# Kernel optimization log

Measured on AMD Instinct MI355X. Metric: run time of the kernel, lower is better.

## Reference

```python
import jax, jax.numpy as jnp
import numpy as np

B, LQ, LK, D = 4, 256, 256, 768


def setup_inputs() -> dict:
    key = jax.random.key(0)
    ks = jax.random.split(key, 11)
    s = 1.0 / np.sqrt(D)
    return {
        "query": jax.random.normal(ks[0], (B, LQ, D), jnp.float32),
        "key": jax.random.normal(ks[1], (B, LK, D), jnp.float32),
        "value": jax.random.normal(ks[2], (B, LK, D), jnp.float32),
        "Wq": jax.random.uniform(ks[3], (D, D), jnp.float32, -s, s),
        "bq": jax.random.uniform(ks[4], (D,), jnp.float32, -s, s),
        "Wk": jax.random.uniform(ks[5], (D, D), jnp.float32, -s, s),
        "bk": jax.random.uniform(ks[6], (D,), jnp.float32, -s, s),
        "Wv": jax.random.uniform(ks[7], (D, D), jnp.float32, -s, s),
        "bv": jax.random.uniform(ks[8], (D,), jnp.float32, -s, s),
        "Ws": jax.random.uniform(ks[9], (D,), jnp.float32, -s, s),
        "bs": jax.random.uniform(ks[10], (), jnp.float32, -s, s),
    }


def reference(query, key, value, Wq, bq, Wk, bk, Wv, bv, Ws, bs):
    # Linear projections (torch Linear: x @ W.T + b; here W stored as [in, out])
    q = jnp.einsum('bqd,de->bqe', query, Wq) + bq   # [B,Lq,D]
    k = jnp.einsum('bkd,de->bke', key, Wk) + bk     # [B,Lk,D]
    v = jnp.einsum('bkd,de->bke', value, Wv) + bv   # [B,Lk,D]
    # Additive (Bahdanau) scores: tanh(q_i + k_j) . Ws + bs  -> [B,Lq,Lk]
    h = jnp.tanh(q[:, :, None, :] + k[:, None, :, :])  # [B,Lq,Lk,D]
    scores = jnp.einsum('bqkd,d->bqk', h, Ws) + bs
    attention_weights = jax.nn.softmax(scores, axis=-1)  # [B,Lq,Lk]
    attended = jnp.einsum('bqk,bkd->bqd', attention_weights, v)
    return attended, attention_weights
```

## Files before the change

kernel.cpp:

```cpp
#include <hip/hip_runtime.h>

#define NB 4
#define SLQ 256
#define SLK 256
#define DD 768

#define TWO_LOG2E 2.8853900817779268f
#define LOG2E 1.4426950408889634f

typedef _Float16 f16x4 __attribute__((ext_vector_type(4)));
typedef _Float16 f16x8 __attribute__((ext_vector_type(8)));
typedef float f32x4 __attribute__((ext_vector_type(4)));

__device__ __forceinline__ float fexp2(float x) { return __builtin_amdgcn_exp2f(x); }
__device__ __forceinline__ float frcp(float x) { return __builtin_amdgcn_rcpf(x); }

#define LSTR 40
#define TSTR 72
#define NPS  ((size_t)NB * SLQ * SLK)

__global__ __launch_bounds__(256) void prep_a_kernel(
    const float* __restrict__ q, const float* __restrict__ k,
    const float* __restrict__ v, _Float16* __restrict__ qh,
    _Float16* __restrict__ kh, _Float16* __restrict__ vh)
{
    const int z = blockIdx.z;
    const float* src = (z == 0) ? q : (z == 1) ? k : v;
    _Float16* dst = (z == 0) ? qh : (z == 1) ? kh : vh;
    const int i8 = (blockIdx.x * 256 + threadIdx.x) * 8;
    float4 a = *(const float4*)&src[i8];
    float4 b = *(const float4*)&src[i8 + 4];
    f16x8 h;
    h[0] = (_Float16)a.x; h[1] = (_Float16)a.y; h[2] = (_Float16)a.z; h[3] = (_Float16)a.w;
    h[4] = (_Float16)b.x; h[5] = (_Float16)b.y; h[6] = (_Float16)b.z; h[7] = (_Float16)b.w;
    *(f16x8*)&dst[i8] = h;
}

__global__ __launch_bounds__(256) void prep_wt_kernel(
    const float* __restrict__ Wq, const float* __restrict__ Wk,
    const float* __restrict__ Wv, _Float16* __restrict__ wtq,
    _Float16* __restrict__ wtk, _Float16* __restrict__ wtv)
{
    const int z = blockIdx.z;
    const float* W = (z == 0) ? Wq : (z == 1) ? Wk : Wv;
    _Float16* Wt = (z == 0) ? wtq : (z == 1) ? wtk : wtv;

    __shared__ float t[64][65];
    const int tid = threadIdx.x;
    const int kt0 = blockIdx.y * 64;
    const int nt0 = blockIdx.x * 64;

    const int col4 = (tid & 15) << 2;
#pragma unroll
    for (int i = 0; i < 4; ++i) {
        const int row = ((tid >> 4) << 2) + i;
        *(float4*)&t[row][col4] = *(const float4*)&W[(size_t)(kt0 + row) * DD + nt0 + col4];
    }
    __syncthreads();
    const int n = tid >> 2;
    const int k16 = (tid & 3) << 4;
    f16x8 h0, h1;
#pragma unroll
    for (int j = 0; j < 8; ++j) {
        h0[j] = (_Float16)t[k16 + j][n];
        h1[j] = (_Float16)t[k16 + 8 + j][n];
    }
    *(f16x8*)&Wt[(size_t)(nt0 + n) * DD + kt0 + k16] = h0;
    *(f16x8*)&Wt[(size_t)(nt0 + n) * DD + kt0 + k16 + 8] = h1;
}

__global__ __launch_bounds__(256) void qkv_f16_kernel(
    const _Float16* __restrict__ qh, const _Float16* __restrict__ kh,
    const _Float16* __restrict__ vh, const _Float16* __restrict__ wtq,
    const _Float16* __restrict__ wtk, const _Float16* __restrict__ wtv,
    const float* __restrict__ bq, const float* __restrict__ bk,
    const float* __restrict__ bv, float* __restrict__ eq,
    _Float16* __restrict__ ekc, _Float16* __restrict__ vsht)
{
    const int z = blockIdx.z;
    const _Float16* A = (z == 0) ? qh : (z == 1) ? kh : vh;
    const _Float16* Wt = (z == 0) ? wtq : (z == 1) ? wtk : wtv;
    const float* bias = (z == 0) ? bq : (z == 1) ? bk : bv;

    __shared__ _Float16 Sh[2][2][64 * LSTR];

    const int tid = threadIdx.x;
    const int lane = tid & 63;
    const int wid = tid >> 6;
    const int wr = wid >> 1;
    const int wc = wid & 1;
    const int row0 = blockIdx.y * 64;
    const int col0 = blockIdx.x * 64;

    const int sr = tid >> 2;
    const int sc = (tid & 3) << 3;

    const _Float16* Ap = A + (size_t)(row0 + sr) * DD + sc;
    const _Float16* Bp = Wt + (size_t)(col0 + sr) * DD + sc;

    f16x8 pa = *(const f16x8*)Ap;
    f16x8 pb = *(const f16x8*)Bp;

    f32x4 acc[2][2] = {};
    const int kj = (lane >> 4) << 3;
    const int fr = lane & 15;

    *(f16x8*)&Sh[0][0][sr * LSTR + sc] = pa;
    *(f16x8*)&Sh[0][1][sr * LSTR + sc] = pb;
    __syncthreads();

    int p = 0;
    for (int s = 0; s < DD / 32; ++s) {
        if (s + 1 < DD / 32) {
            pa = *(const f16x8*)(Ap + (s + 1) * 32);
            pb = *(const f16x8*)(Bp + (s + 1) * 32);
        }
        f16x8 af0 = *(const f16x8*)&Sh[p][0][(wr * 32 + fr) * LSTR + kj];
        f16x8 af1 = *(const f16x8*)&Sh[p][0][(wr * 32 + 16 + fr) * LSTR + kj];
        f16x8 bf0 = *(const f16x8*)&Sh[p][1][(wc * 32 + fr) * LSTR + kj];
        f16x8 bf1 = *(const f16x8*)&Sh[p][1][(wc * 32 + 16 + fr) * LSTR + kj];
        acc[0][0] = __builtin_amdgcn_mfma_f32_16x16x32_f16(af0, bf0, acc[0][0], 0, 0, 0);
        acc[0][1] = __builtin_amdgcn_mfma_f32_16x16x32_f16(af0, bf1, acc[0][1], 0, 0, 0);
        acc[1][0] = __builtin_amdgcn_mfma_f32_16x16x32_f16(af1, bf0, acc[1][0], 0, 0, 0);
        acc[1][1] = __builtin_amdgcn_mfma_f32_16x16x32_f16(af1, bf1, acc[1][1], 0, 0, 0);
        if (s + 1 < DD / 32) {
            *(f16x8*)&Sh[p ^ 1][0][sr * LSTR + sc] = pa;
            *(f16x8*)&Sh[p ^ 1][1][sr * LSTR + sc] = pb;
        }
        __syncthreads();
        p ^= 1;
    }

    const int colb = col0 + wc * 32 + fr;
    const int rowb = row0 + wr * 32 + ((lane >> 4) << 2);

    if (z < 2) {
#pragma unroll
        for (int mf = 0; mf < 2; ++mf) {
#pragma unroll
            for (int nf = 0; nf < 2; ++nf) {
                const int col = colb + nf * 16;
                const float bvv = bias[col];
#pragma unroll
                for (int r = 0; r < 4; ++r) {
                    const int row = rowb + mf * 16 + r;
                    const float arg = fminf((acc[mf][nf][r] + bvv) * TWO_LOG2E, 15.0f);
                    if (z == 0) {
                        eq[(size_t)row * DD + col] = fexp2(arg);
                    } else {
                        const int b = row >> 8, k = row & 255;
                        ekc[(size_t)b * (SLK * DD) + ((col >> 3) * (SLK * 8)) +
                            k * 8 + (col & 7)] = (_Float16)fexp2(arg);
                    }
                }
            }
        }
    } else {
        _Float16* T = (_Float16*)Sh;
#pragma unroll
        for (int mf = 0; mf < 2; ++mf) {
#pragma unroll
            for (int nf = 0; nf < 2; ++nf) {
                const int cl = wc * 32 + fr + nf * 16;
                const float bvv = bias[col0 + cl];
                const int rl = wr * 32 + mf * 16 + ((lane >> 4) << 2);
                f16x4 h;
#pragma unroll
                for (int r = 0; r < 4; ++r) h[r] = (_Float16)(acc[mf][nf][r] + bvv);
                *(f16x4*)&T[cl * TSTR + rl] = h;
            }
        }
        __syncthreads();
        const int b = row0 >> 8;
        const int krow0 = row0 & 255;
#pragma unroll
        for (int j = 0; j < 2; ++j) {
            const int u = tid + 256 * j;
            const int c2 = u >> 3;
            const int g = u & 7;
            f16x8 hv = *(const f16x8*)&T[c2 * TSTR + g * 8];
            *(f16x8*)&vsht[((size_t)b * DD + col0 + c2) * SLK + krow0 + g * 8] = hv;
        }
    }
}

__global__ __launch_bounds__(256) void scores_partial_kernel(
    const float* __restrict__ Eq, const _Float16* __restrict__ Ekc,
    const float* __restrict__ Ws, float* __restrict__ pbuf)
{
    const int bz = blockIdx.z;
    const int b = bz >> 2;
    const int s = bz & 3;
    const int k0 = blockIdx.x * 64;
    const int q0 = blockIdx.y * 8;
    const int lane = threadIdx.x & 63;
    const int wid = __builtin_amdgcn_readfirstlane((int)(threadIdx.x >> 6));
    const int q = q0 + (wid << 1);
    const int d0 = s * 192;

    const _Float16* kr = Ekc + (size_t)b * (SLK * DD) + ((d0 >> 3) * (SLK * 8)) +
                         (k0 + lane) * 8;
    const float* qp0 = Eq + (size_t)(b * SLQ + q) * DD + d0;
    const float* qp1 = qp0 + DD;
    const float* wp = Ws + d0;

    float acc0 = 0.f, acc1 = 0.f;

#pragma unroll 4
    for (int c = 0; c < 24; ++c) {
        const int dn = c * 8;
        f16x8 e = *(const f16x8*)(kr + (size_t)c * (SLK * 8));
        float4 ga0 = *(const float4*)(qp0 + dn);
        float4 ga1 = *(const float4*)(qp0 + dn + 4);
        float4 gb0 = *(const float4*)(qp1 + dn);
        float4 gb1 = *(const float4*)(qp1 + dn + 4);
        float4 w0 = *(const float4*)(wp + dn);
        float4 w1 = *(const float4*)(wp + dn + 4);

        float e0 = (float)e[0], e1 = (float)e[1], e2 = (float)e[2], e3 = (float)e[3];
        float e4 = (float)e[4], e5 = (float)e[5], e6 = (float)e[6], e7 = (float)e[7];

        acc0 = fmaf(w0.x, frcp(fmaf(ga0.x, e0, 1.0f)), acc0);
        acc1 = fmaf(w0.x, frcp(fmaf(gb0.x, e0, 1.0f)), acc1);
        acc0 = fmaf(w0.y, frcp(fmaf(ga0.y, e1, 1.0f)), acc0);
        acc1 = fmaf(w0.y, frcp(fmaf(gb0.y, e1, 1.0f)), acc1);
        acc0 = fmaf(w0.z, frcp(fmaf(ga0.z, e2, 1.0f)), acc0);
        acc1 = fmaf(w0.z, frcp(fmaf(gb0.z, e2, 1.0f)), acc1);
        acc0 = fmaf(w0.w, frcp(fmaf(ga0.w, e3, 1.0f)), acc0);
        acc1 = fmaf(w0.w, frcp(fmaf(gb0.w, e3, 1.0f)), acc1);
        acc0 = fmaf(w1.x, frcp(fmaf(ga1.x, e4, 1.0f)), acc0);
        acc1 = fmaf(w1.x, frcp(fmaf(gb1.x, e4, 1.0f)), acc1);
        acc0 = fmaf(w1.y, frcp(fmaf(ga1.y, e5, 1.0f)), acc0);
        acc1 = fmaf(w1.y, frcp(fmaf(gb1.y, e5, 1.0f)), acc1);
        acc0 = fmaf(w1.z, frcp(fmaf(ga1.z, e6, 1.0f)), acc0);
        acc1 = fmaf(w1.z, frcp(fmaf(gb1.z, e6, 1.0f)), acc1);
        acc0 = fmaf(w1.w, frcp(fmaf(ga1.w, e7, 1.0f)), acc0);
        acc1 = fmaf(w1.w, frcp(fmaf(gb1.w, e7, 1.0f)), acc1);
    }

    const size_t o = (size_t)s * NPS + (size_t)(b * SLQ + q) * SLK + k0 + lane;
    pbuf[o] = -2.0f * acc0;
    pbuf[o + SLK] = -2.0f * acc1;
}

__global__ __launch_bounds__(256) void softmax_combine_kernel(
    const float* __restrict__ pbuf, float* __restrict__ attnw,
    _Float16* __restrict__ phalf)
{
    const int lane = threadIdx.x & 63;
    const int wv = threadIdx.x >> 6;
    const int row = blockIdx.x * 4 + wv;
    const size_t base = (size_t)row * SLK + (lane << 2);

    float4 x0 = *(const float4*)&pbuf[base];
    float4 x1 = *(const float4*)&pbuf[base + NPS];
    float4 x2 = *(const float4*)&pbuf[base + 2 * NPS];
    float4 x3 = *(const float4*)&pbuf[base + 3 * NPS];
    float4 x;
    x.x = (x0.x + x1.x) + (x2.x + x3.x);
    x.y = (x0.y + x1.y) + (x2.y + x3.y);
    x.z = (x0.z + x1.z) + (x2.z + x3.z);
    x.w = (x0.w + x1.w) + (x2.w + x3.w);

    float m = fmaxf(fmaxf(x.x, x.y), fmaxf(x.z, x.w));
#pragma unroll
    for (int off = 32; off; off >>= 1) m = fmaxf(m, __shfl_xor(m, off, 64));

    float e0 = fexp2((x.x - m) * LOG2E);
    float e1 = fexp2((x.y - m) * LOG2E);
    float e2 = fexp2((x.z - m) * LOG2E);
    float e3 = fexp2((x.w - m) * LOG2E);
    float sm = (e0 + e1) + (e2 + e3);
#pragma unroll
    for (int off = 32; off; off >>= 1) sm += __shfl_xor(sm, off, 64);

    const float inv = 1.0f / sm;
    float4 o;
    o.x = e0 * inv; o.y = e1 * inv; o.z = e2 * inv; o.w = e3 * inv;
    *(float4*)&attnw[base] = o;

    f16x4 h;
    h[0] = (_Float16)o.x; h[1] = (_Float16)o.y;
    h[2] = (_Float16)o.z; h[3] = (_Float16)o.w;
    *(f16x4*)&phalf[base] = h;
}

__global__ __launch_bounds__(256) void attended_f16_kernel(
    const _Float16* __restrict__ phalf, const _Float16* __restrict__ vsht,
    float* __restrict__ out)
{
    const int b = blockIdx.z;
    const _Float16* A = phalf + (size_t)b * SLQ * SLK;
    const _Float16* Bt = vsht + (size_t)b * DD * SLK;
    float* C = out + (size_t)b * SLQ * DD;

    __shared__ _Float16 Sh[2][2][64 * LSTR];

    const int tid = threadIdx.x;
    const int lane = tid & 63;
    const int wid = tid >> 6;
    const int wr = wid >> 1;
    const int wc = wid & 1;
    const int row0 = blockIdx.y * 64;
    const int col0 = blockIdx.x * 64;

    const int sr = tid >> 2;
    const int sc = (tid & 3) << 3;

    const _Float16* Ap = A + (size_t)(row0 + sr) * SLK + sc;
    const _Float16* Bp = Bt + (size_t)(col0 + sr) * SLK + sc;

    f16x8 pa = *(const f16x8*)Ap;
    f16x8 pb = *(const f16x8*)Bp;

    f32x4 acc[2][2] = {};
    const int kj = (lane >> 4) << 3;
    const int fr = lane & 15;

    *(f16x8*)&Sh[0][0][sr * LSTR + sc] = pa;
    *(f16x8*)&Sh[0][1][sr * LSTR + sc] = pb;
    __syncthreads();

    int p = 0;
    for (int s = 0; s < SLK / 32; ++s) {
        if (s + 1 < SLK / 32) {
            pa = *(const f16x8*)(Ap + (s + 1) * 32);
            pb = *(const f16x8*)(Bp + (s + 1) * 32);
        }
        f16x8 af0 = *(const f16x8*)&Sh[p][0][(wr * 32 + fr) * LSTR + kj];
        f16x8 af1 = *(const f16x8*)&Sh[p][0][(wr * 32 + 16 + fr) * LSTR + kj];
        f16x8 bf0 = *(const f16x8*)&Sh[p][1][(wc * 32 + fr) * LSTR + kj];
        f16x8 bf1 = *(const f16x8*)&Sh[p][1][(wc * 32 + 16 + fr) * LSTR + kj];
        acc[0][0] = __builtin_amdgcn_mfma_f32_16x16x32_f16(af0, bf0, acc[0][0], 0, 0, 0);
        acc[0][1] = __builtin_amdgcn_mfma_f32_16x16x32_f16(af0, bf1, acc[0][1], 0, 0, 0);
        acc[1][0] = __builtin_amdgcn_mfma_f32_16x16x32_f16(af1, bf0, acc[1][0], 0, 0, 0);
        acc[1][1] = __builtin_amdgcn_mfma_f32_16x16x32_f16(af1, bf1, acc[1][1], 0, 0, 0);
        if (s + 1 < SLK / 32) {
            *(f16x8*)&Sh[p ^ 1][0][sr * LSTR + sc] = pa;
            *(f16x8*)&Sh[p ^ 1][1][sr * LSTR + sc] = pb;
        }
        __syncthreads();
        p ^= 1;
    }

    const int colb = col0 + wc * 32 + fr;
    const int rowb = row0 + wr * 32 + ((lane >> 4) << 2);
#pragma unroll
    for (int mf = 0; mf < 2; ++mf)
#pragma unroll
        for (int nf = 0; nf < 2; ++nf)
#pragma unroll
            for (int r = 0; r < 4; ++r)
                C[(size_t)(rowb + mf * 16 + r) * DD + colb + nf * 16] = acc[mf][nf][r];
}

extern "C" void kernel_launch(void* const* d_in, const int* in_sizes, int n_in,
                              void* d_out, int out_size, void* d_ws, size_t ws_size,
                              hipStream_t stream)
{
    (void)in_sizes; (void)n_in; (void)out_size; (void)ws_size;

    const float* query = (const float*)d_in[0];
    const float* key   = (const float*)d_in[1];
    const float* value = (const float*)d_in[2];
    const float* Wq = (const float*)d_in[3];
    const float* bq = (const float*)d_in[4];
    const float* Wk = (const float*)d_in[5];
    const float* bk = (const float*)d_in[6];
    const float* Wv = (const float*)d_in[7];
    const float* bv = (const float*)d_in[8];
    const float* Ws = (const float*)d_in[9];

    const size_t NE = (size_t)NB * SLQ * DD;
    const size_t NW = (size_t)DD * DD;

    char* w = (char*)d_ws;
    float* eq = (float*)w;               w += NE * 4;
    _Float16* ekc = (_Float16*)w;        w += NE * 2;
    _Float16* vsht = (_Float16*)w;       w += NE * 2;
    _Float16* phalf = (_Float16*)w;      w += NPS * 2;
    _Float16* qh = (_Float16*)w;         w += NE * 2;
    _Float16* kh = (_Float16*)w;         w += NE * 2;
    _Float16* vh = (_Float16*)w;         w += NE * 2;
    _Float16* wtq = (_Float16*)w;        w += NW * 2;
    _Float16* wtk = (_Float16*)w;        w += NW * 2;
    _Float16* wtv = (_Float16*)w;        w += NW * 2;
    float* pbuf = (float*)w;

    float* out = (float*)d_out;
    float* attended = out;
    float* attnw = out + NE;

    prep_a_kernel<<<dim3(NE / (256 * 8), 1, 3), 256, 0, stream>>>(
        query, key, value, qh, kh, vh);
    prep_wt_kernel<<<dim3(DD / 64, DD / 64, 3), 256, 0, stream>>>(
        Wq, Wk, Wv, wtq, wtk, wtv);
    qkv_f16_kernel<<<dim3(DD / 64, (NB * SLQ) / 64, 3), 256, 0, stream>>>(
        qh, kh, vh, wtq, wtk, wtv, bq, bk, bv, eq, ekc, vsht);
    scores_partial_kernel<<<dim3(SLK / 64, SLQ / 8, NB * 4), 256, 0, stream>>>(
        eq, ekc, Ws, pbuf);
    softmax_combine_kernel<<<dim3((NB * SLQ) / 4), 256, 0, stream>>>(
        pbuf, attnw, phalf);
    attended_f16_kernel<<<dim3(DD / 64, SLQ / 64, NB), 256, 0, stream>>>(
        phalf, vsht, attended);
}
```

Baseline: 133.0 us.

## Fuse input fp16 conversion into QKV GEMM, stage epilogue, pair reciprocals, retile attended

Removes the separate input-to-fp16 prep kernel so the QKV GEMM loads fp32 inputs and converts them while staging into shared memory. The GEMM epilogue now writes through a shared-memory tile, giving coalesced vector stores for eq and the chunked ekc layout instead of scattered scalar stores. In the score kernel, pairs of reciprocals are merged into one reciprocal of a product, which roughly halves rcp instructions at the cost of extra multiplies and some overflow risk. The attended GEMM uses 64x32 tiles over a flattened batch so it launches more blocks.

```diff
diff --git a/kernel.cpp b/kernel.cpp
--- a/kernel.cpp
+++ b/kernel.cpp
@@ -17,24 +17,8 @@
 
 #define LSTR 40
 #define TSTR 72
+#define TFSTR 65
 #define NPS  ((size_t)NB * SLQ * SLK)
-
-__global__ __launch_bounds__(256) void prep_a_kernel(
-    const float* __restrict__ q, const float* __restrict__ k,
-    const float* __restrict__ v, _Float16* __restrict__ qh,
-    _Float16* __restrict__ kh, _Float16* __restrict__ vh)
-{
-    const int z = blockIdx.z;
-    const float* src = (z == 0) ? q : (z == 1) ? k : v;
-    _Float16* dst = (z == 0) ? qh : (z == 1) ? kh : vh;
-    const int i8 = (blockIdx.x * 256 + threadIdx.x) * 8;
-    float4 a = *(const float4*)&src[i8];
-    float4 b = *(const float4*)&src[i8 + 4];
-    f16x8 h;
-    h[0] = (_Float16)a.x; h[1] = (_Float16)a.y; h[2] = (_Float16)a.z; h[3] = (_Float16)a.w;
-    h[4] = (_Float16)b.x; h[5] = (_Float16)b.y; h[6] = (_Float16)b.z; h[7] = (_Float16)b.w;
-    *(f16x8*)&dst[i8] = h;
-}
 
 __global__ __launch_bounds__(256) void prep_wt_kernel(
     const float* __restrict__ Wq, const float* __restrict__ Wk,
@@ -70,15 +54,15 @@
 }
 
 __global__ __launch_bounds__(256) void qkv_f16_kernel(
-    const _Float16* __restrict__ qh, const _Float16* __restrict__ kh,
-    const _Float16* __restrict__ vh, const _Float16* __restrict__ wtq,
+    const float* __restrict__ query, const float* __restrict__ key_in,
+    const float* __restrict__ value, const _Float16* __restrict__ wtq,
     const _Float16* __restrict__ wtk, const _Float16* __restrict__ wtv,
     const float* __restrict__ bq, const float* __restrict__ bk,
     const float* __restrict__ bv, float* __restrict__ eq,
     _Float16* __restrict__ ekc, _Float16* __restrict__ vsht)
 {
     const int z = blockIdx.z;
-    const _Float16* A = (z == 0) ? qh : (z == 1) ? kh : vh;
+    const float* A = (z == 0) ? query : (z == 1) ? key_in : value;
     const _Float16* Wt = (z == 0) ? wtq : (z == 1) ? wtk : wtv;
     const float* bias = (z == 0) ? bq : (z == 1) ? bk : bv;
 
@@ -95,24 +79,33 @@
     const int sr = tid >> 2;
     const int sc = (tid & 3) << 3;
 
-    const _Float16* Ap = A + (size_t)(row0 + sr) * DD + sc;
+    const float* Ap = A + (size_t)(row0 + sr) * DD + sc;
     const _Float16* Bp = Wt + (size_t)(col0 + sr) * DD + sc;
 
-    f16x8 pa = *(const f16x8*)Ap;
+    float4 pa0 = *(const float4*)Ap;
+    float4 pa1 = *(const float4*)(Ap + 4);
     f16x8 pb = *(const f16x8*)Bp;
 
     f32x4 acc[2][2] = {};
     const int kj = (lane >> 4) << 3;
     const int fr = lane & 15;
 
-    *(f16x8*)&Sh[0][0][sr * LSTR + sc] = pa;
-    *(f16x8*)&Sh[0][1][sr * LSTR + sc] = pb;
+    {
+        f16x8 ha;
+        ha[0] = (_Float16)pa0.x; ha[1] = (_Float16)pa0.y;
+        ha[2] = (_Float16)pa0.z; ha[3] = (_Float16)pa0.w;
+        ha[4] = (_Float16)pa1.x; ha[5] = (_Float16)pa1.y;
+        ha[6] = (_Float16)pa1.z; ha[7] = (_Float16)pa1.w;
+        *(f16x8*)&Sh[0][0][sr * LSTR + sc] = ha;
+        *(f16x8*)&Sh[0][1][sr * LSTR + sc] = pb;
+    }
     __syncthreads();
 
     int p = 0;
     for (int s = 0; s < DD / 32; ++s) {
         if (s + 1 < DD / 32) {
-            pa = *(const f16x8*)(Ap + (s + 1) * 32);
+            pa0 = *(const float4*)(Ap + (s + 1) * 32);
+            pa1 = *(const float4*)(Ap + (s + 1) * 32 + 4);
             pb = *(const f16x8*)(Bp + (s + 1) * 32);
         }
         f16x8 af0 = *(const f16x8*)&Sh[p][0][(wr * 32 + fr) * LSTR + kj];
@@ -124,46 +117,72 @@
         acc[1][0] = __builtin_amdgcn_mfma_f32_16x16x32_f16(af1, bf0, acc[1][0], 0, 0, 0);
         acc[1][1] = __builtin_amdgcn_mfma_f32_16x16x32_f16(af1, bf1, acc[1][1], 0, 0, 0);
         if (s + 1 < DD / 32) {
-            *(f16x8*)&Sh[p ^ 1][0][sr * LSTR + sc] = pa;
+            f16x8 ha;
+            ha[0] = (_Float16)pa0.x; ha[1] = (_Float16)pa0.y;
+            ha[2] = (_Float16)pa0.z; ha[3] = (_Float16)pa0.w;
+            ha[4] = (_Float16)pa1.x; ha[5] = (_Float16)pa1.y;
+            ha[6] = (_Float16)pa1.z; ha[7] = (_Float16)pa1.w;
+            *(f16x8*)&Sh[p ^ 1][0][sr * LSTR + sc] = ha;
             *(f16x8*)&Sh[p ^ 1][1][sr * LSTR + sc] = pb;
         }
         __syncthreads();
         p ^= 1;
     }
 
-    const int colb = col0 + wc * 32 + fr;
-    const int rowb = row0 + wr * 32 + ((lane >> 4) << 2);
+    const int clb = wc * 32 + fr;
+    const int rlb = wr * 32 + ((lane >> 4) << 2);
 
     if (z < 2) {
+        float* Tf = (float*)Sh;
 #pragma unroll
         for (int mf = 0; mf < 2; ++mf) {
 #pragma unroll
             for (int nf = 0; nf < 2; ++nf) {
-                const int col = colb + nf * 16;
-                const float bvv = bias[col];
+                const int cl = clb + nf * 16;
+                const float bvv = bias[col0 + cl];
 #pragma unroll
                 for (int r = 0; r < 4; ++r) {
-                    const int row = rowb + mf * 16 + r;
+                    const int rl = rlb + mf * 16 + r;
                     const float arg = fminf((acc[mf][nf][r] + bvv) * TWO_LOG2E, 15.0f);
-                    if (z == 0) {
-                        eq[(size_t)row * DD + col] = fexp2(arg);
-                    } else {
-                        const int b = row >> 8, k = row & 255;
-                        ekc[(size_t)b * (SLK * DD) + ((col >> 3) * (SLK * 8)) +
-                            k * 8 + (col & 7)] = (_Float16)fexp2(arg);
-                    }
+                    Tf[rl * TFSTR + cl] = fexp2(arg);
                 }
             }
         }
+        __syncthreads();
+        if (z == 0) {
+#pragma unroll
+            for (int j = 0; j < 4; ++j) {
+                const int u = tid + j * 256;
+                const int row = u >> 4;
+                const int c4 = (u & 15) << 2;
+                float4 v = *(const float4*)&Tf[row * TFSTR + c4];
+                *(float4*)&eq[(size_t)(row0 + row) * DD + col0 + c4] = v;
+            }
+        } else {
+            const int b = row0 >> 8;
+            const int krow0 = row0 & 255;
+            const size_t base = (size_t)b * (SLK * DD) + (size_t)(col0 >> 3) * (SLK * 8);
+#pragma unroll
+            for (int j = 0; j < 2; ++j) {
+                const int u = tid + j * 256;
+                const int c2 = u >> 6;
+                const int k = u & 63;
+                const float* src = &Tf[k * TFSTR + c2 * 8];
+                f16x8 h;
+#pragma unroll
+                for (int i = 0; i < 8; ++i) h[i] = (_Float16)src[i];
+                *(f16x8*)&ekc[base + (size_t)c2 * (SLK * 8) + (size_t)(krow0 + k) * 8] = h;
+            }
+        }
     } else {
         _Float16* T = (_Float16*)Sh;
 #pragma unroll
         for (int mf = 0; mf < 2; ++mf) {
 #pragma unroll
             for (int nf = 0; nf < 2; ++nf) {
-                const int cl = wc * 32 + fr + nf * 16;
+                const int cl = clb + nf * 16;
                 const float bvv = bias[col0 + cl];
-                const int rl = wr * 32 + mf * 16 + ((lane >> 4) << 2);
+                const int rl = rlb + mf * 16;
                 f16x4 h;
 #pragma unroll
                 for (int r = 0; r < 4; ++r) h[r] = (_Float16)(acc[mf][nf][r] + bvv);
@@ -220,22 +239,26 @@
         float e0 = (float)e[0], e1 = (float)e[1], e2 = (float)e[2], e3 = (float)e[3];
         float e4 = (float)e[4], e5 = (float)e[5], e6 = (float)e[6], e7 = (float)e[7];
 
-        acc0 = fmaf(w0.x, frcp(fmaf(ga0.x, e0, 1.0f)), acc0);
-        acc1 = fmaf(w0.x, frcp(fmaf(gb0.x, e0, 1.0f)), acc1);
-        acc0 = fmaf(w0.y, frcp(fmaf(ga0.y, e1, 1.0f)), acc0);
-        acc1 = fmaf(w0.y, frcp(fmaf(gb0.y, e1, 1.0f)), acc1);
-        acc0 = fmaf(w0.z, frcp(fmaf(ga0.z, e2, 1.0f)), acc0);
-        acc1 = fmaf(w0.z, frcp(fmaf(gb0.z, e2, 1.0f)), acc1);
-        acc0 = fmaf(w0.w, frcp(fmaf(ga0.w, e3, 1.0f)), acc0);
-        acc1 = fmaf(w0.w, frcp(fmaf(gb0.w, e3, 1.0f)), acc1);
-        acc0 = fmaf(w1.x, frcp(fmaf(ga1.x, e4, 1.0f)), acc0);
-        acc1 = fmaf(w1.x, frcp(fmaf(gb1.x, e4, 1.0f)), acc1);
-        acc0 = fmaf(w1.y, frcp(fmaf(ga1.y, e5, 1.0f)), acc0);
-        acc1 = fmaf(w1.y, frcp(fmaf(gb1.y, e5, 1.0f)), acc1);
-        acc0 = fmaf(w1.z, frcp(fmaf(ga1.z, e6, 1.0f)), acc0);
-        acc1 = fmaf(w1.z, frcp(fmaf(gb1.z, e6, 1.0f)), acc1);
-        acc0 = fmaf(w1.w, frcp(fmaf(ga1.w, e7, 1.0f)), acc0);
-        acc1 = fmaf(w1.w, frcp(fmaf(gb1.w, e7, 1.0f)), acc1);
+        {
+            float A0 = fmaf(ga0.x, e0, 1.0f), A1 = fmaf(ga0.y, e1, 1.0f);
+            float A2 = fmaf(ga0.z, e2, 1.0f), A3 = fmaf(ga0.w, e3, 1.0f);
+            float A4 = fmaf(ga1.x, e4, 1.0f), A5 = fmaf(ga1.y, e5, 1.0f);
+            float A6 = fmaf(ga1.z, e6, 1.0f), A7 = fmaf(ga1.w, e7, 1.0f);
+            acc0 = fmaf(fmaf(w0.x, A1, w0.y * A0), frcp(A0 * A1), acc0);
+            acc0 = fmaf(fmaf(w0.z, A3, w0.w * A2), frcp(A2 * A3), acc0);
+            acc0 = fmaf(fmaf(w1.x, A5, w1.y * A4), frcp(A4 * A5), acc0);
+            acc0 = fmaf(fmaf(w1.z, A7, w1.w * A6), frcp(A6 * A7), acc0);
+        }
+        {
+            float A0 = fmaf(gb0.x, e0, 1.0f), A1 = fmaf(gb0.y, e1, 1.0f);
+            float A2 = fmaf(gb0.z, e2, 1.0f), A3 = fmaf(gb0.w, e3, 1.0f);
+            float A4 = fmaf(gb1.x, e4, 1.0f), A5 = fmaf(gb1.y, e5, 1.0f);
+            float A6 = fmaf(gb1.z, e6, 1.0f), A7 = fmaf(gb1.w, e7, 1.0f);
+            acc1 = fmaf(fmaf(w0.x, A1, w0.y * A0), frcp(A0 * A1), acc1);
+            acc1 = fmaf(fmaf(w0.z, A3, w0.w * A2), frcp(A2 * A3), acc1);
+            acc1 = fmaf(fmaf(w1.x, A5, w1.y * A4), frcp(A4 * A5), acc1);
+            acc1 = fmaf(fmaf(w1.z, A7, w1.w * A6), frcp(A6 * A7), acc1);
+        }
     }
 
     const size_t o = (size_t)s * NPS + (size_t)(b * SLQ + q) * SLK + k0 + lane;
@@ -289,69 +312,65 @@
     const _Float16* __restrict__ phalf, const _Float16* __restrict__ vsht,
     float* __restrict__ out)
 {
-    const int b = blockIdx.z;
-    const _Float16* A = phalf + (size_t)b * SLQ * SLK;
+    const int row0 = blockIdx.y * 64;
+    const int col0 = blockIdx.x * 32;
+    const int b = row0 >> 8;
     const _Float16* Bt = vsht + (size_t)b * DD * SLK;
-    float* C = out + (size_t)b * SLQ * DD;
-
-    __shared__ _Float16 Sh[2][2][64 * LSTR];
+    float* C = out + (size_t)(row0)*DD;
+
+    __shared__ _Float16 Ah[2][64 * LSTR];
+    __shared__ _Float16 Bh[2][32 * LSTR];
 
     const int tid = threadIdx.x;
     const int lane = tid & 63;
     const int wid = tid >> 6;
-    const int wr = wid >> 1;
-    const int wc = wid & 1;
-    const int row0 = blockIdx.y * 64;
-    const int col0 = blockIdx.x * 64;
 
     const int sr = tid >> 2;
     const int sc = (tid & 3) << 3;
-
-    const _Float16* Ap = A + (size_t)(row0 + sr) * SLK + sc;
-    const _Float16* Bp = Bt + (size_t)(col0 + sr) * SLK + sc;
+    const int br = tid >> 2;
+    const int bc = (tid & 3) << 3;
+
+    const _Float16* Ap = phalf + (size_t)(row0 + sr) * SLK + sc;
+    const _Float16* Bp = Bt + (size_t)(col0 + br) * SLK + bc;
 
     f16x8 pa = *(const f16x8*)Ap;
-    f16x8 pb = *(const f16x8*)Bp;
-
-    f32x4 acc[2][2] = {};
+    f16x8 pb;
+    if (tid < 128) pb = *(const f16x8*)Bp;
+
+    f32x4 acc0 = {}, acc1 = {};
     const int kj = (lane >> 4) << 3;
     const int fr = lane & 15;
 
-    *(f16x8*)&Sh[0][0][sr * LSTR + sc] = pa;
-    *(f16x8*)&Sh[0][1][sr * LSTR + sc] = pb;
+    *(f16x8*)&Ah[0][sr * LSTR + sc] = pa;
+    if (tid < 128) *(f16x8*)&Bh[0][br * LSTR + bc] = pb;
     __syncthreads();
 
     int p = 0;
     for (int s = 0; s < SLK / 32; ++s) {
         if (s + 1 < SLK / 32) {
             pa = *(const f16x8*)(Ap + (s + 1) * 32);
-            pb = *(const f16x8*)(Bp + (s + 1) * 32);
-        }
-        f16x8 af0 = *(const f16x8*)&Sh[p][0][(wr * 32 + fr) * LSTR + kj];
-        f16x8 af1 = *(const f16x8*)&Sh[p][0][(wr * 32 + 16 + fr) * LSTR + kj];
-        f16x8 bf0 = *(const f16x8*)&Sh[p][1][(wc * 32 + fr) * LSTR + kj];
-        f16x8 bf1 = *(const f16x8*)&Sh[p][1][(wc * 32 + 16 + fr) * LSTR + kj];
-        acc[0][0] = __builtin_amdgcn_mfma_f32_16x16x32_f16(af0, bf0, acc[0][0], 0, 0, 0);
-        acc[0][1] = __builtin_amdgcn_mfma_f32_16x16x32_f16(af0, bf1, acc[0][1], 0, 0, 0);
-        acc[1][0] = __builtin_amdgcn_mfma_f32_16x16x32_f16(af1, bf0, acc[1][0], 0, 0, 0);
-        acc[1][1] = __builtin_amdgcn_mfma_f32_16x16x32_f16(af1, bf1, acc[1][1], 0, 0, 0);
+            if (tid < 128) pb = *(const f16x8*)(Bp + (s + 1) * 32);
+        }
+        f16x8 af = *(const f16x8*)&Ah[p][(wid * 16 + fr) * LSTR + kj];
+        f16x8 bf0 = *(const f16x8*)&Bh[p][fr * LSTR + kj];
+        f16x8 bf1 = *(const f16x8*)&Bh[p][(16 + fr) * LSTR + kj];
+        acc0 = __builtin_amdgcn_mfma_f32_16x16x32_f16(af, bf0, acc0, 0, 0, 0);
+        acc1 = __builtin_amdgcn_mfma_f32_16x16x32_f16(af, bf1, acc1, 0, 0, 0);
         if (s + 1 < SLK / 32) {
-            *(f16x8*)&Sh[p ^ 1][0][sr * LSTR + sc] = pa;
-            *(f16x8*)&Sh[p ^ 1][1][sr * LSTR + sc] = pb;
+            *(f16x8*)&Ah[p ^ 1][sr * LSTR + sc] = pa;
+            if (tid < 128) *(f16x8*)&Bh[p ^ 1][br * LSTR + bc] = pb;
         }
         __syncthreads();
         p ^= 1;
     }
 
-    const int colb = col0 + wc * 32 + fr;
-    const int rowb = row0 + wr * 32 + ((lane >> 4) << 2);
-#pragma unroll
-    for (int mf = 0; mf < 2; ++mf)
-#pragma unroll
-        for (int nf = 0; nf < 2; ++nf)
-#pragma unroll
-            for (int r = 0; r < 4; ++r)
-                C[(size_t)(rowb + mf * 16 + r) * DD + colb + nf * 16] = acc[mf][nf][r];
+    const int colb = col0 + fr;
+    const int rowb = wid * 16 + ((lane >> 4) << 2);
+#pragma unroll
+    for (int r = 0; r < 4; ++r) {
+        C[(size_t)(rowb + r) * DD + colb] = acc0[r];
+        C[(size_t)(rowb + r) * DD + colb + 16] = acc1[r];
+    }
 }
 
 extern "C" void kernel_launch(void* const* d_in, const int* in_sizes, int n_in,
@@ -379,9 +398,6 @@
     _Float16* ekc = (_Float16*)w;        w += NE * 2;
     _Float16* vsht = (_Float16*)w;       w += NE * 2;
     _Float16* phalf = (_Float16*)w;      w += NPS * 2;
-    _Float16* qh = (_Float16*)w;         w += NE * 2;
-    _Float16* kh = (_Float16*)w;         w += NE * 2;
-    _Float16* vh = (_Float16*)w;         w += NE * 2;
     _Float16* wtq = (_Float16*)w;        w += NW * 2;
     _Float16* wtk = (_Float16*)w;        w += NW * 2;
     _Float16* wtv = (_Float16*)w;        w += NW * 2;
@@ -391,16 +407,14 @@
     float* attended = out;
     float* attnw = out + NE;
 
-    prep_a_kernel<<<dim3(NE / (256 * 8), 1, 3), 256, 0, stream>>>(
-        query, key, value, qh, kh, vh);
     prep_wt_kernel<<<dim3(DD / 64, DD / 64, 3), 256, 0, stream>>>(
         Wq, Wk, Wv, wtq, wtk, wtv);
     qkv_f16_kernel<<<dim3(DD / 64, (NB * SLQ) / 64, 3), 256, 0, stream>>>(
-        qh, kh, vh, wtq, wtk, wtv, bq, bk, bv, eq, ekc, vsht);
+        query, key, value, wtq, wtk, wtv, bq, bk, bv, eq, ekc, vsht);
     scores_partial_kernel<<<dim3(SLK / 64, SLQ / 8, NB * 4), 256, 0, stream>>>(
         eq, ekc, Ws, pbuf);
     softmax_combine_kernel<<<dim3((NB * SLQ) / 4), 256, 0, stream>>>(
         pbuf, attnw, phalf);
-    attended_f16_kernel<<<dim3(DD / 64, SLQ / 64, NB), 256, 0, stream>>>(
+    attended_f16_kernel<<<dim3(DD / 32, (NB * SLQ) / 64, 1), 256, 0, stream>>>(
         phalf, vsht, attended);
 }
```

Result: no change. 133.4 us (+0.3%).
